# Performance work log

Measured on AMD Instinct MI355X. Metric: run time of the kernel, lower is better.

Reference implementation:

```python
import jax, jax.numpy as jnp
import numpy as np
import math


def setup_inputs() -> dict:
    key = jax.random.key(0)
    k_fm, k_x, k_y, k_w, k_h = jax.random.split(key, 5)
    C, H, W = 512, 256, 256
    N = 4096
    patch_num = 4
    pe = 2  # sqrt(patch_num)
    feature_map = jax.random.normal(k_fm, (C, H, W), dtype=jnp.float32)
    # Boxes fully inside the map with per-patch extent >= 2 so every sub-box is valid.
    min_wh = 2.0 * pe + 1.0
    x0 = jax.random.uniform(k_x, (N,), minval=0.0, maxval=W / 2 - 1.0)
    y0 = jax.random.uniform(k_y, (N,), minval=0.0, maxval=H / 2 - 1.0)
    w = jax.random.uniform(k_w, (N,), minval=min_wh, maxval=W / 2 - 2.0)
    h = jax.random.uniform(k_h, (N,), minval=min_wh, maxval=H / 2 - 2.0)
    roi_batch = jnp.stack([x0, y0, x0 + w, y0 + h], axis=1).astype(jnp.float32)
    return {"feature_map": feature_map, "roi_batch": roi_batch, "patch_num": patch_num}


def _box_indices(roi_batch, patch_num, W):
    """Rounded, clamped per-patch sub-box corners; shapes (P, N), flattened patch-major."""
    pe = int(math.isqrt(patch_num))
    xmin, ymin, xmax, ymax = (roi_batch[:, k] for k in range(4))
    i = jnp.arange(patch_num)
    ix = (i % pe).astype(roi_batch.dtype)[:, None]
    iy = (i // pe).astype(roi_batch.dtype)[:, None]
    ws = ((xmax - xmin) / pe)[None, :]
    hs = ((ymax - ymin) / pe)[None, :]
    ax = xmin[None, :] + ix * ws  # (P, N)
    ay = ymin[None, :] + iy * hs
    clampi = lambda v: jnp.clip(jnp.round(v), 0, W - 1).astype(jnp.int32)
    x0, x1 = clampi(ax), clampi(ax + ws)
    y0, y1 = clampi(ay), clampi(ay + hs)
    flat = lambda a: a.reshape(-1)  # loop order: patch outer, roi inner
    return flat(x0), flat(x1), flat(y0), flat(y1)


def reference(feature_map, roi_batch, patch_num):
    C, H, W = feature_map.shape
    x0, x1, y0, y1 = _box_indices(roi_batch, patch_num, W)
    cw = x1 - x0
    ch = y1 - y0
    mask = (cw >= 1) & (ch >= 1)  # (P*N,)
    # Integral image with zero row/col padding: S[:, y, x] = sum of fm[:, :y, :x]
    S = jnp.pad(jnp.cumsum(jnp.cumsum(feature_map, axis=1), axis=2),
                ((0, 0), (1, 0), (1, 0)))
    # Region sums via 4-corner gather: (C, B)
    sums = S[:, y1, x1] - S[:, y0, x1] - S[:, y1, x0] + S[:, y0, x0]
    area = jnp.maximum(cw * ch, 1).astype(feature_map.dtype)
    pooled = (sums / area).T  # (B, C) region means == adaptive_avg_pool2d(.,(1,1))
    pooled = pooled * mask.astype(feature_map.dtype)[:, None]
    return pooled[:, :, None, None], mask.astype(jnp.int32)
```

## Files before the change

### kernel.cpp

```cpp
#include <hip/hip_runtime.h>


#define CHN   512
#define HDIM  256
#define WDIM  256
#define SP    257
#define PADW  260

__global__ __launch_bounds__(256) void zeroK(float* __restrict__ S) {
    int gid = blockIdx.x * 256 + threadIdx.x;
    const int half = SP * CHN;
    if (gid < half) {
        S[gid] = 0.0f;
    } else {
        int g2 = gid - half;
        if (g2 < half) {
            int y = g2 >> 9;
            int c = g2 & 511;
            S[((size_t)y * SP) * CHN + c] = 0.0f;
        }
    }
}

__global__ __launch_bounds__(256) void rowScanK(const float* __restrict__ fm,
                                               float* __restrict__ S) {
    __shared__ float tile[32][PADW];
    const int t    = threadIdx.x;
    const int lane = t & 63;
    const int wave = t >> 6;
    const int y    = blockIdx.x;
    const int c0   = blockIdx.y * 32;

    #pragma unroll
    for (int cc = 0; cc < 8; ++cc) {
        const int c = wave * 8 + cc;
        const float4 v = *(const float4*)(fm + ((size_t)(c0 + c) << 16)
                                             + ((size_t)y << 8) + 4 * lane);
        const float local = ((v.x + v.y) + v.z) + v.w;
        float s = local;
        #pragma unroll
        for (int d = 1; d < 64; d <<= 1) {
            float u = __shfl_up(s, d, 64);
            if (lane >= d) s += u;
        }
        const float e  = s - local;
        float4 p;
        p.x = e   + v.x;
        p.y = p.x + v.y;
        p.z = p.y + v.z;
        p.w = p.z + v.w;
        *(float4*)&tile[c][4 * lane] = p;
    }
    __syncthreads();

    #pragma unroll
    for (int it = 0; it < 8; ++it) {
        const int lin = it * 256 + t;
        const int cg  = lin & 7;
        const int x   = lin >> 3;
        float4 o;
        o.x = tile[cg * 4 + 0][x];
        o.y = tile[cg * 4 + 1][x];
        o.z = tile[cg * 4 + 2][x];
        o.w = tile[cg * 4 + 3][x];
        *(float4*)(S + (((size_t)(y + 1)) * SP + (x + 1)) * CHN + c0 + cg * 4) = o;
    }
}

__global__ __launch_bounds__(256) void colScanK(float* __restrict__ S) {
    const int g = blockIdx.x * 256 + threadIdx.x;
    const int c = g & 511;
    const int x = (g >> 9) + 1;
    const size_t stride = (size_t)SP * CHN;
    size_t idx = ((size_t)SP + x) * CHN + c;

    float buf[16];
    #pragma unroll
    for (int i = 0; i < 16; ++i) buf[i] = S[idx + (size_t)i * stride];

    double acc = 0.0;
    for (int yb = 0; yb < 16; ++yb) {
        float nbuf[16];
        const size_t nidx = idx + 16 * stride;
        if (yb < 15) {
            #pragma unroll
            for (int i = 0; i < 16; ++i) nbuf[i] = S[nidx + (size_t)i * stride];
        }
        #pragma unroll
        for (int i = 0; i < 16; ++i) {
            acc += (double)buf[i];
            S[idx + (size_t)i * stride] = (float)acc;
        }
        idx = nidx;
        #pragma unroll
        for (int i = 0; i < 16; ++i) buf[i] = nbuf[i];
    }
}

__global__ __launch_bounds__(128) void gatherK(const float* __restrict__ S,
                                              const float* __restrict__ roi,
                                              float* __restrict__ out,
                                              float* __restrict__ maskOut,
                                              int N) {
    const int n = blockIdx.x >> 2;
    const int p = blockIdx.x & 3;
    const int b = p * N + n;

    const float xmin = roi[4 * n + 0];
    const float ymin = roi[4 * n + 1];
    const float xmax = roi[4 * n + 2];
    const float ymax = roi[4 * n + 3];

    const float ixf = (float)(p & 1);
    const float iyf = (float)(p >> 1);
    const float wsv = __fdiv_rn(__fsub_rn(xmax, xmin), 2.0f);
    const float hsv = __fdiv_rn(__fsub_rn(ymax, ymin), 2.0f);
    const float ax  = __fadd_rn(xmin, __fmul_rn(ixf, wsv));
    const float ay  = __fadd_rn(ymin, __fmul_rn(iyf, hsv));

    const float lim = (float)(WDIM - 1);
    float f;
    f = fminf(fmaxf(rintf(ax), 0.0f), lim);                     const int x0 = (int)f;
    f = fminf(fmaxf(rintf(__fadd_rn(ax, wsv)), 0.0f), lim);     const int x1 = (int)f;
    f = fminf(fmaxf(rintf(ay), 0.0f), lim);                     const int y0 = (int)f;
    f = fminf(fmaxf(rintf(__fadd_rn(ay, hsv)), 0.0f), lim);     const int y1 = (int)f;

    const int cw = x1 - x0;
    const int ch = y1 - y0;
    const int maskv = (cw >= 1 && ch >= 1) ? 1 : 0;
    int areai = cw * ch; if (areai < 1) areai = 1;
    const float areaf = (float)areai;
    const float maskf = (float)maskv;

    const float4* p11 = (const float4*)(S + ((size_t)y1 * SP + x1) * CHN);
    const float4* p01 = (const float4*)(S + ((size_t)y0 * SP + x1) * CHN);
    const float4* p10 = (const float4*)(S + ((size_t)y1 * SP + x0) * CHN);
    const float4* p00 = (const float4*)(S + ((size_t)y0 * SP + x0) * CHN);
    float4* ob = (float4*)(out + (size_t)b * CHN);

    const int t = threadIdx.x;
    const float4 a = p11[t];
    const float4 bq = p01[t];
    const float4 cq = p10[t];
    const float4 dq = p00[t];
    float4 o;
    o.x = __fdiv_rn(((a.x - bq.x) - cq.x) + dq.x, areaf) * maskf;
    o.y = __fdiv_rn(((a.y - bq.y) - cq.y) + dq.y, areaf) * maskf;
    o.z = __fdiv_rn(((a.z - bq.z) - cq.z) + dq.z, areaf) * maskf;
    o.w = __fdiv_rn(((a.w - bq.w) - cq.w) + dq.w, areaf) * maskf;
    ob[t] = o;

    if (t == 0) maskOut[b] = maskf;
}

extern "C" void kernel_launch(void* const* d_in, const int* in_sizes, int n_in,
                              void* d_out, int out_size, void* d_ws, size_t ws_size,
                              hipStream_t stream) {
    const float* fm  = (const float*)d_in[0];
    const float* roi = (const float*)d_in[1];

    const int N = in_sizes[1] / 4;
    const int B = 4 * N;

    float* S       = (float*)d_ws;
    float* out     = (float*)d_out;
    float* maskOut = out + (size_t)B * CHN;

    zeroK<<<(2 * SP * CHN + 255) / 256, 256, 0, stream>>>(S);

    dim3 gA(HDIM, CHN / 32);
    rowScanK<<<gA, 256, 0, stream>>>(fm, S);

    colScanK<<<(WDIM * CHN) / 256, 256, 0, stream>>>(S);

    gatherK<<<B, 128, 0, stream>>>(S, roi, out, maskOut, N);
}
```

Measured before the change: 284.0 us.

## Share corner loads across patches in gather and fold zeroing into row scan

The gather kernel now processes all four patches of an ROI in one block and loads the 3x3 shared corner grid once, instead of 16 separate corner loads. Each thread now handles float2 channels. The separate zeroing kernel is removed, and its work is done inside the row-scan kernel, saving a launch and a pass over memory. The trade-offs are more register pressure in the gather and narrower per-thread loads.

Result: faster. 275.9 us (-2.9%).

```diff
diff --git a/kernel.cpp b/kernel.cpp
--- a/kernel.cpp
+++ b/kernel.cpp
@@ -7,21 +7,6 @@
 #define SP    257
 #define PADW  260
 
-__global__ __launch_bounds__(256) void zeroK(float* __restrict__ S) {
-    int gid = blockIdx.x * 256 + threadIdx.x;
-    const int half = SP * CHN;
-    if (gid < half) {
-        S[gid] = 0.0f;
-    } else {
-        int g2 = gid - half;
-        if (g2 < half) {
-            int y = g2 >> 9;
-            int c = g2 & 511;
-            S[((size_t)y * SP) * CHN + c] = 0.0f;
-        }
-    }
-}
-
 __global__ __launch_bounds__(256) void rowScanK(const float* __restrict__ fm,
                                                float* __restrict__ S) {
     __shared__ float tile[32][PADW];
@@ -30,6 +15,20 @@
     const int wave = t >> 6;
     const int y    = blockIdx.x;
     const int c0   = blockIdx.y * 32;
+
+    const float4 z4 = make_float4(0.f, 0.f, 0.f, 0.f);
+    if (t < 8) {
+        *(float4*)(S + ((size_t)(y + 1) * SP) * CHN + c0 + 4 * t) = z4;
+    }
+    if (y == 0) {
+        #pragma unroll
+        for (int it = 0; it < 8; ++it) {
+            const int lin = it * 256 + t;
+            const int cg  = lin & 7;
+            const int x   = lin >> 3;
+            *(float4*)(S + (size_t)x * CHN + c0 + cg * 4) = z4;
+        }
+    }
 
     #pragma unroll
     for (int cc = 0; cc < 8; ++cc) {
@@ -97,60 +96,61 @@
     }
 }
 
-__global__ __launch_bounds__(128) void gatherK(const float* __restrict__ S,
+__global__ __launch_bounds__(256) void gatherK(const float* __restrict__ S,
                                               const float* __restrict__ roi,
                                               float* __restrict__ out,
                                               float* __restrict__ maskOut,
                                               int N) {
-    const int n = blockIdx.x >> 2;
-    const int p = blockIdx.x & 3;
-    const int b = p * N + n;
-
+    const int n = blockIdx.x;
     const float xmin = roi[4 * n + 0];
     const float ymin = roi[4 * n + 1];
     const float xmax = roi[4 * n + 2];
     const float ymax = roi[4 * n + 3];
 
-    const float ixf = (float)(p & 1);
-    const float iyf = (float)(p >> 1);
     const float wsv = __fdiv_rn(__fsub_rn(xmax, xmin), 2.0f);
     const float hsv = __fdiv_rn(__fsub_rn(ymax, ymin), 2.0f);
-    const float ax  = __fadd_rn(xmin, __fmul_rn(ixf, wsv));
-    const float ay  = __fadd_rn(ymin, __fmul_rn(iyf, hsv));
+    const float ax1 = __fadd_rn(xmin, wsv);
+    const float ay1 = __fadd_rn(ymin, hsv);
+    const float lim = (float)(WDIM - 1);
 
-    const float lim = (float)(WDIM - 1);
-    float f;
-    f = fminf(fmaxf(rintf(ax), 0.0f), lim);                     const int x0 = (int)f;
-    f = fminf(fmaxf(rintf(__fadd_rn(ax, wsv)), 0.0f), lim);     const int x1 = (int)f;
-    f = fminf(fmaxf(rintf(ay), 0.0f), lim);                     const int y0 = (int)f;
-    f = fminf(fmaxf(rintf(__fadd_rn(ay, hsv)), 0.0f), lim);     const int y1 = (int)f;
-
-    const int cw = x1 - x0;
-    const int ch = y1 - y0;
-    const int maskv = (cw >= 1 && ch >= 1) ? 1 : 0;
-    int areai = cw * ch; if (areai < 1) areai = 1;
-    const float areaf = (float)areai;
-    const float maskf = (float)maskv;
-
-    const float4* p11 = (const float4*)(S + ((size_t)y1 * SP + x1) * CHN);
-    const float4* p01 = (const float4*)(S + ((size_t)y0 * SP + x1) * CHN);
-    const float4* p10 = (const float4*)(S + ((size_t)y1 * SP + x0) * CHN);
-    const float4* p00 = (const float4*)(S + ((size_t)y0 * SP + x0) * CHN);
-    float4* ob = (float4*)(out + (size_t)b * CHN);
+    int rx[3], ry[3];
+    rx[0] = (int)fminf(fmaxf(rintf(xmin), 0.0f), lim);
+    rx[1] = (int)fminf(fmaxf(rintf(ax1), 0.0f), lim);
+    rx[2] = (int)fminf(fmaxf(rintf(__fadd_rn(ax1, wsv)), 0.0f), lim);
+    ry[0] = (int)fminf(fmaxf(rintf(ymin), 0.0f), lim);
+    ry[1] = (int)fminf(fmaxf(rintf(ay1), 0.0f), lim);
+    ry[2] = (int)fminf(fmaxf(rintf(__fadd_rn(ay1, hsv)), 0.0f), lim);
 
     const int t = threadIdx.x;
-    const float4 a = p11[t];
-    const float4 bq = p01[t];
-    const float4 cq = p10[t];
-    const float4 dq = p00[t];
-    float4 o;
-    o.x = __fdiv_rn(((a.x - bq.x) - cq.x) + dq.x, areaf) * maskf;
-    o.y = __fdiv_rn(((a.y - bq.y) - cq.y) + dq.y, areaf) * maskf;
-    o.z = __fdiv_rn(((a.z - bq.z) - cq.z) + dq.z, areaf) * maskf;
-    o.w = __fdiv_rn(((a.w - bq.w) - cq.w) + dq.w, areaf) * maskf;
-    ob[t] = o;
+    float2 g[3][3];
+    #pragma unroll
+    for (int j = 0; j < 3; ++j)
+        #pragma unroll
+        for (int i = 0; i < 3; ++i)
+            g[j][i] = *(const float2*)(S + ((size_t)ry[j] * SP + rx[i]) * CHN + 2 * t);
 
-    if (t == 0) maskOut[b] = maskf;
+    float m[4];
+    #pragma unroll
+    for (int p = 0; p < 4; ++p) {
+        const int ix = p & 1, iy = p >> 1;
+        const int cw = rx[ix + 1] - rx[ix];
+        const int ch = ry[iy + 1] - ry[iy];
+        const int maskv = (cw >= 1 && ch >= 1) ? 1 : 0;
+        int areai = cw * ch; if (areai < 1) areai = 1;
+        const float areaf = (float)areai;
+        const float maskf = (float)maskv;
+        m[p] = maskf;
+
+        const float2 s11 = g[iy + 1][ix + 1];
+        const float2 s01 = g[iy][ix + 1];
+        const float2 s10 = g[iy + 1][ix];
+        const float2 s00 = g[iy][ix];
+        float2 o;
+        o.x = __fdiv_rn(((s11.x - s01.x) - s10.x) + s00.x, areaf) * maskf;
+        o.y = __fdiv_rn(((s11.y - s01.y) - s10.y) + s00.y, areaf) * maskf;
+        *(float2*)(out + ((size_t)p * N + n) * CHN + 2 * t) = o;
+    }
+    if (t < 4) maskOut[(size_t)t * N + n] = m[t];
 }
 
 extern "C" void kernel_launch(void* const* d_in, const int* in_sizes, int n_in,
@@ -166,12 +166,10 @@
     float* out     = (float*)d_out;
     float* maskOut = out + (size_t)B * CHN;
 
-    zeroK<<<(2 * SP * CHN + 255) / 256, 256, 0, stream>>>(S);
-
     dim3 gA(HDIM, CHN / 32);
     rowScanK<<<gA, 256, 0, stream>>>(fm, S);
 
     colScanK<<<(WDIM * CHN) / 256, 256, 0, stream>>>(S);
 
-    gatherK<<<B, 128, 0, stream>>>(S, roi, out, maskOut, N);
+    gatherK<<<N, 256, 0, stream>>>(S, roi, out, maskOut, N);
 }
```
